# Kernel optimization log

Hardware: AMD Instinct MI355X
Metric: run time of the kernel (lower is better)

The kernel has to match this reference:

```python
import jax, jax.numpy as jnp
import numpy as np

B, S, D, E, K = 4, 2048, 1024, 8, 2


def setup_inputs() -> dict:
    key = jax.random.key(0)
    k1, k2, k3 = jax.random.split(key, 3)
    scale = 1.0 / np.sqrt(D)
    x = jax.random.normal(k1, (B, S, D), dtype=jnp.float32)
    Wg = jax.random.normal(k2, (D, E), dtype=jnp.float32) * scale
    bg = jnp.zeros((E,), dtype=jnp.float32)
    We = jax.random.normal(k3, (E, D, D), dtype=jnp.float32) * scale
    be = jnp.zeros((E, D), dtype=jnp.float32)
    return {"x": x, "Wg": Wg, "bg": bg, "We": We, "be": be}


def reference(x, Wg, bg, We, be):
    # gate scores: [B, S, E]
    gate_scores = jnp.einsum("bsd,de->bse", x, Wg) + bg
    topk_values, topk_indices = jax.lax.top_k(gate_scores, K)
    # mask: -inf everywhere except at top-k indices (where value == score)
    sel = jax.nn.one_hot(topk_indices, E, dtype=jnp.bool_).any(axis=-2)  # [B,S,E]
    masked = jnp.where(sel, gate_scores, -jnp.inf)
    gate_weights = jax.nn.softmax(masked, axis=-1)  # [B,S,E]
    # dense all-expert compute, as in the original: [B,S,E,D]
    expert_outputs = jnp.einsum("bsd,edh->bseh", x, We) + be
    fused = jnp.einsum("bse,bseh->bsh", gate_weights, expert_outputs)
    return fused
```

## Files before the change

kernel.cpp:

```cpp
#include <hip/hip_runtime.h>
#include <stdint.h>

#define NTOK   8192
#define DIM    1024
#define NEXP   8
#define MAXP   8192

#define BM 128
#define BN 128
#define BK 32

typedef float    f32x4  __attribute__((ext_vector_type(4)));
typedef __bf16   bf16x8 __attribute__((ext_vector_type(8)));
typedef _Float16 h16x8  __attribute__((ext_vector_type(8)));

typedef __attribute__((address_space(1))) const void* gas_ptr;
typedef __attribute__((address_space(3))) void*       las_ptr;

__device__ __forceinline__ unsigned short f32_to_bf16(float f) {
  union { float f; unsigned int u; } v; v.f = f;
  unsigned int u = v.u;
  unsigned int r = (u + 0x7FFFu + ((u >> 16) & 1u)) >> 16;
  return (unsigned short)r;
}

__global__ __launch_bounds__(256) void prep_kernel(
    const float* __restrict__ We, unsigned short* __restrict__ Wf,
    const float* __restrict__ x, const float* __restrict__ Wg,
    const float* __restrict__ bg, unsigned short* __restrict__ Xbf,
    int* __restrict__ tok_ee, float2* __restrict__ tok_w) {
  __shared__ float tile[64][65];
  const int bid = blockIdx.x;
  if (bid < 2048) {
    const int e  = bid >> 8;
    const int d0 = ((bid >> 4) & 15) * 64;
    const int h0 = (bid & 15) * 64;
    const int t  = threadIdx.x;
    const int tx = t & 63, ty = t >> 6;
    const float* src = We + (size_t)e * DIM * DIM;
#pragma unroll
    for (int i = 0; i < 16; ++i) {
      int d = ty + i * 4;
      tile[d][tx] = src[(size_t)(d0 + d) * DIM + (h0 + tx)];
    }
    __syncthreads();
    const int nt    = h0 >> 7;
    const int rbase = h0 & 64;
    const int hl    = t >> 2;
    const int k8    = t & 3;
#pragma unroll
    for (int reg = 0; reg < 2; ++reg) {
      const int kt = (d0 >> 5) + reg;
      unsigned int pk[4];
#pragma unroll
      for (int q = 0; q < 4; ++q) {
        int dl = reg * 32 + k8 * 8 + q * 2;
        pk[q] = (unsigned int)f32_to_bf16(tile[dl][hl]) |
                ((unsigned int)f32_to_bf16(tile[dl + 1][hl]) << 16);
      }
      size_t base = (((size_t)(e * 8 + nt) * 32 + kt) << 12) +
                    (size_t)(rbase + hl) * 32 + k8 * 8;
      *(uint4*)&Wf[base] = make_uint4(pk[0], pk[1], pk[2], pk[3]);
    }
    return;
  }
  const int blk  = bid - 2048;
  const int wave = threadIdx.x >> 6;
  const int lane = threadIdx.x & 63;
  const int tok0 = blk * 16 + wave * 4;

  float xs[4][16];
#pragma unroll
  for (int t = 0; t < 4; ++t) {
    const float* xr = x + (size_t)(tok0 + t) * DIM + lane * 16;
#pragma unroll
    for (int i = 0; i < 4; ++i)
      *(f32x4*)&xs[t][i * 4] = *(const f32x4*)(xr + i * 4);
  }
#pragma unroll
  for (int t = 0; t < 4; ++t) {
    unsigned int pk[8];
#pragma unroll
    for (int i = 0; i < 8; ++i)
      pk[i] = (unsigned int)f32_to_bf16(xs[t][2 * i]) |
              ((unsigned int)f32_to_bf16(xs[t][2 * i + 1]) << 16);
    uint4* xb = (uint4*)(Xbf + (size_t)(tok0 + t) * DIM + lane * 16);
    xb[0] = make_uint4(pk[0], pk[1], pk[2], pk[3]);
    xb[1] = make_uint4(pk[4], pk[5], pk[6], pk[7]);
  }

  double acc[4][8];
#pragma unroll
  for (int t = 0; t < 4; ++t)
#pragma unroll
    for (int e = 0; e < 8; ++e) acc[t][e] = 0.0;

  const float* wr = Wg + (size_t)(lane * 16) * NEXP;
#pragma unroll
  for (int i = 0; i < 16; ++i) {
    f32x4 wa = *(const f32x4*)(wr + i * 8);
    f32x4 wb = *(const f32x4*)(wr + i * 8 + 4);
    double w0 = wa[0], w1 = wa[1], w2 = wa[2], w3 = wa[3];
    double w4 = wb[0], w5 = wb[1], w6 = wb[2], w7 = wb[3];
#pragma unroll
    for (int t = 0; t < 4; ++t) {
      double xd = (double)xs[t][i];
      acc[t][0] += xd * w0; acc[t][1] += xd * w1;
      acc[t][2] += xd * w2; acc[t][3] += xd * w3;
      acc[t][4] += xd * w4; acc[t][5] += xd * w5;
      acc[t][6] += xd * w6; acc[t][7] += xd * w7;
    }
  }
#pragma unroll
  for (int m = 1; m < 64; m <<= 1)
#pragma unroll
    for (int t = 0; t < 4; ++t)
#pragma unroll
      for (int e = 0; e < 8; ++e) acc[t][e] += __shfl_xor(acc[t][e], m, 64);

  if (lane == 0) {
#pragma unroll
    for (int t = 0; t < 4; ++t) {
      float s[8];
#pragma unroll
      for (int e = 0; e < 8; ++e) s[e] = (float)acc[t][e] + bg[e];
      int i0 = 0; float v0 = s[0];
#pragma unroll
      for (int e = 1; e < 8; ++e) if (s[e] > v0) { v0 = s[e]; i0 = e; }
      int i1 = -1; float v1 = -3.4e38f;
#pragma unroll
      for (int e = 0; e < 8; ++e) if (e != i0 && s[e] > v1) { v1 = s[e]; i1 = e; }
      float t1 = expf(v1 - v0);
      float den = 1.0f + t1;
      tok_ee[tok0 + t] = i0 | (i1 << 8);
      tok_w[tok0 + t]  = make_float2(1.0f / den, t1 / den);
    }
  }
}

__global__ __launch_bounds__(1024) void compact_kernel(
    const int* __restrict__ tok_ee, const float2* __restrict__ tok_w,
    int* __restrict__ counts, int* __restrict__ pair_token,
    float* __restrict__ pair_w) {
  __shared__ int wave_cnt[16];
  __shared__ int wave_off[16];
  const int e = blockIdx.x;
  const int tid = threadIdx.x, wave = tid >> 6, lane = tid & 63;
  int base = 0;
  for (int c = 0; c < NTOK / 1024; ++c) {
    const int t = c * 1024 + tid;
    const int p = tok_ee[t];
    const bool m0 = ((p & 255) == e);
    const bool m1 = (((p >> 8) & 255) == e);
    const unsigned long long m = __ballot(m0 || m1);
    const int pre = __popcll(m & ((1ull << lane) - 1ull));
    if (lane == 0) wave_cnt[wave] = __popcll(m);
    __syncthreads();
    if (tid == 0) {
      int s = base;
      for (int w = 0; w < 16; ++w) { wave_off[w] = s; s += wave_cnt[w]; }
      base = s;
    }
    __syncthreads();
    if (m0 || m1) {
      const float2 w = tok_w[t];
      const int slot = wave_off[wave] + pre;
      pair_token[e * MAXP + slot] = (t << 1) | (m1 ? 1 : 0);
      pair_w[e * MAXP + slot]     = m1 ? w.y : w.x;
    }
    __syncthreads();
  }
  if (tid == 0) counts[e] = base;
}

__global__ __launch_bounds__(256) void moe_gemm(
    const unsigned short* __restrict__ Xbf, const unsigned short* __restrict__ Wf,
    const float* __restrict__ be, const int* __restrict__ counts,
    const int* __restrict__ pair_token, const float* __restrict__ pair_w,
    _Float16* __restrict__ part, float* __restrict__ Y, int use_part) {
  const int id  = blockIdx.x;
  const int e   = id & 7;
  const int nt  = (id >> 3) & 7;
  const int n0  = nt * BN;
  const int m0  = (id >> 6) * BM;
  const int cnt = counts[e];
  if (m0 >= cnt) return;

  __shared__ __align__(16) unsigned short As[3][BM * BK];
  __shared__ __align__(16) unsigned short Bs[3][BN * BK];

  const int tid  = threadIdx.x;
  const int wave = tid >> 6;
  const int lane = tid & 63;
  const int fm   = lane & 15;
  const int fq   = lane >> 4;
  const int wm   = wave >> 1;
  const int wn   = wave & 1;

  const int srow = wave * 32 + (lane >> 2);
  const int kc   = (((lane & 3) ^ ((lane >> 3) & 3)) * 8);
  const unsigned short* gA[2];
#pragma unroll
  for (int c = 0; c < 2; ++c) {
    int r  = srow + c * 16;
    int gr = m0 + r;
    int tk = (gr < cnt) ? (pair_token[e * MAXP + gr] >> 1) : 0;
    gA[c] = Xbf + (size_t)tk * DIM + kc;
  }
  const unsigned short* gB = Wf + (((size_t)(e * 8 + nt) * 32) << 12) +
                             (wave * 2) * 512 + (lane >> 2) * 32 + kc;

#define STAGE(buf, k0v)                                                       \
  {                                                                           \
    _Pragma("unroll") for (int c = 0; c < 2; ++c) {                           \
      __builtin_amdgcn_global_load_lds(                                       \
          (gas_ptr)(uintptr_t)(gA[c] + (k0v)),                                \
          (las_ptr)(uintptr_t)(&As[buf][(wave * 2 + c) * 512]), 16, 0, 0);    \
      __builtin_amdgcn_global_load_lds(                                       \
          (gas_ptr)(uintptr_t)(gB + (size_t)(k0v) * 128 + c * 512),           \
          (las_ptr)(uintptr_t)(&Bs[buf][(wave * 2 + c) * 512]), 16, 0, 0);    \
    }                                                                         \
  }

  f32x4 acc[4][4];
#pragma unroll
  for (int i = 0; i < 4; ++i)
#pragma unroll
    for (int j = 0; j < 4; ++j) { f32x4 z = {0.f, 0.f, 0.f, 0.f}; acc[i][j] = z; }

  const int ks = ((fq ^ ((fm >> 1) & 3)) * 8);

  STAGE(0, 0);
  STAGE(1, BK);
  int cur = 0;
  for (int k0 = 0; k0 < DIM; k0 += BK) {
    asm volatile("s_waitcnt vmcnt(4)" ::: "memory");
    __builtin_amdgcn_s_barrier();

    int kn = k0 + 2 * BK;
    if (kn >= DIM) kn = 0;
    int nb = cur + 2;
    if (nb >= 3) nb -= 3;
    STAGE(nb, kn);

    bf16x8 af[4], bfr[4];
#pragma unroll
    for (int i = 0; i < 4; ++i)
      af[i] = *(const bf16x8*)&As[cur][(wm * 64 + i * 16 + fm) * BK + ks];
#pragma unroll
    for (int j = 0; j < 4; ++j)
      bfr[j] = *(const bf16x8*)&Bs[cur][(wn * 64 + j * 16 + fm) * BK + ks];
#pragma unroll
    for (int i = 0; i < 4; ++i)
#pragma unroll
      for (int j = 0; j < 4; ++j)
        acc[i][j] = __builtin_amdgcn_mfma_f32_16x16x32_bf16(af[i], bfr[j],
                                                            acc[i][j], 0, 0, 0);
    cur = (cur + 1 == 3) ? 0 : cur + 1;
  }
#undef STAGE

  int   rowv[4][4];
  float wrow[4][4];
#pragma unroll
  for (int i = 0; i < 4; ++i)
#pragma unroll
    for (int r = 0; r < 4; ++r) {
      int gr = m0 + wm * 64 + i * 16 + fq * 4 + r;
      bool valid = gr < cnt;
      rowv[i][r] = valid ? pair_token[e * MAXP + gr] : -1;
      wrow[i][r] = valid ? pair_w[e * MAXP + gr] : 0.f;
    }
  if (use_part) {
#pragma unroll
    for (int j = 0; j < 4; ++j) {
      int col = n0 + wn * 64 + j * 16 + fm;
      float bev = be[e * DIM + col];
#pragma unroll
      for (int i = 0; i < 4; ++i)
#pragma unroll
        for (int r = 0; r < 4; ++r) {
          int v = rowv[i][r];
          if (v >= 0)
            __builtin_nontemporal_store(
                (_Float16)(wrow[i][r] * (acc[i][j][r] + bev)),
                &part[(size_t)v * DIM + col]);
        }
    }
  } else {
#pragma unroll
    for (int j = 0; j < 4; ++j) {
      int col = n0 + wn * 64 + j * 16 + fm;
      float bev = be[e * DIM + col];
#pragma unroll
      for (int i = 0; i < 4; ++i)
#pragma unroll
        for (int r = 0; r < 4; ++r) {
          int v = rowv[i][r];
          if (v >= 0)
            atomicAdd(Y + (size_t)(v >> 1) * DIM + col,
                      wrow[i][r] * (acc[i][j][r] + bev));
        }
    }
  }
}

__global__ __launch_bounds__(256) void reduce_pairs(
    const _Float16* __restrict__ part, float* __restrict__ Y) {
  const int g = blockIdx.x * 256 + threadIdx.x;
  const int t = g >> 7;
  const int o = (g & 127) * 8;
  const h16x8 a =
      __builtin_nontemporal_load((const h16x8*)(part + (size_t)(2 * t) * DIM + o));
  const h16x8 b =
      __builtin_nontemporal_load((const h16x8*)(part + (size_t)(2 * t + 1) * DIM + o));
  float* y = Y + (size_t)t * DIM + o;
  f32x4 lo = {(float)a[0] + (float)b[0], (float)a[1] + (float)b[1],
              (float)a[2] + (float)b[2], (float)a[3] + (float)b[3]};
  f32x4 hi = {(float)a[4] + (float)b[4], (float)a[5] + (float)b[5],
              (float)a[6] + (float)b[6], (float)a[7] + (float)b[7]};
  __builtin_nontemporal_store(lo, (f32x4*)y);
  __builtin_nontemporal_store(hi, (f32x4*)(y + 4));
}

extern "C" void kernel_launch(void* const* d_in, const int* in_sizes, int n_in,
                              void* d_out, int out_size, void* d_ws, size_t ws_size,
                              hipStream_t stream) {
  const float* x  = (const float*)d_in[0];
  const float* Wg = (const float*)d_in[1];
  const float* bg = (const float*)d_in[2];
  const float* We = (const float*)d_in[3];
  const float* be = (const float*)d_in[4];
  float* Y = (float*)d_out;

  const size_t MB = 1024 * 1024;
  char* ws = (char*)d_ws;
  unsigned short* Xbf = (unsigned short*)ws;
  unsigned short* Wf  = (unsigned short*)(ws + 16 * MB);
  const size_t part_bytes = (size_t)NTOK * 2 * DIM * 2;
  const size_t need = 32 * MB + part_bytes + 1 * MB;
  const int use_part = ws_size >= need;
  _Float16* part = (_Float16*)(ws + 32 * MB);
  char* p2 = ws + 32 * MB + (use_part ? part_bytes : 0);
  int*    counts     = (int*)p2;
  int*    pair_token = (int*)(p2 + 256);
  float*  pair_w     = (float*)(p2 + 256 + 262144);
  int*    tok_ee     = (int*)(p2 + 256 + 2 * 262144);
  float2* tok_w      = (float2*)(p2 + 256 + 2 * 262144 + 32768);

  if (!use_part)
    hipMemsetAsync(d_out, 0, (size_t)out_size * sizeof(float), stream);

  prep_kernel<<<2560, 256, 0, stream>>>(We, Wf, x, Wg, bg, Xbf, tok_ee, tok_w);
  compact_kernel<<<NEXP, 1024, 0, stream>>>(tok_ee, tok_w, counts, pair_token,
                                            pair_w);
  moe_gemm<<<8 * 8 * (NTOK / BM), 256, 0, stream>>>(
      Xbf, Wf, be, counts, pair_token, pair_w, part, Y, use_part);
  if (use_part)
    reduce_pairs<<<NTOK * DIM / 8 / 256, 256, 0, stream>>>(part, Y);
}
```

Baseline: 221.2 us.

## Enlarge MoE GEMM tiles to 256x256 with 8 waves and ping-pong pipelining

```diff
diff --git a/kernel.cpp b/kernel.cpp
--- a/kernel.cpp
+++ b/kernel.cpp
@@ -5,10 +5,6 @@
 #define DIM    1024
 #define NEXP   8
 #define MAXP   8192
-
-#define BM 128
-#define BN 128
-#define BK 32
 
 typedef float    f32x4  __attribute__((ext_vector_type(4)));
 typedef __bf16   bf16x8 __attribute__((ext_vector_type(8)));
@@ -173,100 +169,149 @@
   if (tid == 0) counts[e] = base;
 }
 
-__global__ __launch_bounds__(256) void moe_gemm(
+#define BARC()                                  \
+  { asm volatile("" ::: "memory");              \
+    __builtin_amdgcn_s_barrier();               \
+    asm volatile("" ::: "memory"); }
+
+__global__ __launch_bounds__(512, 2) void moe_gemm(
     const unsigned short* __restrict__ Xbf, const unsigned short* __restrict__ Wf,
     const float* __restrict__ be, const int* __restrict__ counts,
     const int* __restrict__ pair_token, const float* __restrict__ pair_w,
     _Float16* __restrict__ part, float* __restrict__ Y, int use_part) {
-  const int id  = blockIdx.x;
-  const int e   = id & 7;
-  const int nt  = (id >> 3) & 7;
-  const int n0  = nt * BN;
-  const int m0  = (id >> 6) * BM;
-  const int cnt = counts[e];
+  const int id    = blockIdx.x;
+  const int e     = id & 7;
+  const int ntile = (id >> 3) & 3;
+  const int m0    = (id >> 5) * 256;
+  const int cnt   = counts[e];
   if (m0 >= cnt) return;
 
-  __shared__ __align__(16) unsigned short As[3][BM * BK];
-  __shared__ __align__(16) unsigned short Bs[3][BN * BK];
+  __shared__ __align__(16) unsigned short As[2][2][256 * 32];
+  __shared__ __align__(16) unsigned short Bs[2][2][256 * 32];
 
   const int tid  = threadIdx.x;
   const int wave = tid >> 6;
   const int lane = tid & 63;
   const int fm   = lane & 15;
   const int fq   = lane >> 4;
-  const int wm   = wave >> 1;
-  const int wn   = wave & 1;
-
-  const int srow = wave * 32 + (lane >> 2);
-  const int kc   = (((lane & 3) ^ ((lane >> 3) & 3)) * 8);
+  const int wm   = wave >> 2;
+  const int wn   = wave & 3;
+
+  const int kc = (((lane & 3) ^ ((lane >> 3) & 3)) * 8);
   const unsigned short* gA[2];
-#pragma unroll
-  for (int c = 0; c < 2; ++c) {
-    int r  = srow + c * 16;
-    int gr = m0 + r;
-    int tk = (gr < cnt) ? (pair_token[e * MAXP + gr] >> 1) : 0;
-    gA[c] = Xbf + (size_t)tk * DIM + kc;
-  }
-  const unsigned short* gB = Wf + (((size_t)(e * 8 + nt) * 32) << 12) +
-                             (wave * 2) * 512 + (lane >> 2) * 32 + kc;
-
-#define STAGE(buf, k0v)                                                       \
-  {                                                                           \
-    _Pragma("unroll") for (int c = 0; c < 2; ++c) {                           \
+  const unsigned short* gB[2];
+#pragma unroll
+  for (int l = 0; l < 2; ++l) {
+    const int R  = wave * 2 + l;
+    const int gr = m0 + R * 16 + (lane >> 2);
+    const int tk = (gr < cnt) ? (pair_token[e * MAXP + gr] >> 1) : 0;
+    gA[l] = Xbf + (size_t)tk * DIM + kc;
+    gB[l] = Wf + ((size_t)(e * 8 + ntile * 2 + (R >> 3)) << 17) +
+            (size_t)((R & 7) * 16 + (lane >> 2)) * 32 + kc;
+  }
+
+#define STAGE_A(buf, ksv, ttv)                                                \
+  { _Pragma("unroll") for (int l = 0; l < 2; ++l)                             \
       __builtin_amdgcn_global_load_lds(                                       \
-          (gas_ptr)(uintptr_t)(gA[c] + (k0v)),                                \
-          (las_ptr)(uintptr_t)(&As[buf][(wave * 2 + c) * 512]), 16, 0, 0);    \
+          (gas_ptr)(uintptr_t)(gA[l] + (ttv) * 64 + (ksv) * 32),              \
+          (las_ptr)(uintptr_t)(&As[buf][ksv][(wave * 2 + l) * 512]), 16, 0, 0); }
+#define STAGE_B(buf, ksv, ttv)                                                \
+  { _Pragma("unroll") for (int l = 0; l < 2; ++l)                             \
       __builtin_amdgcn_global_load_lds(                                       \
-          (gas_ptr)(uintptr_t)(gB + (size_t)(k0v) * 128 + c * 512),           \
-          (las_ptr)(uintptr_t)(&Bs[buf][(wave * 2 + c) * 512]), 16, 0, 0);    \
-    }                                                                         \
-  }
-
-  f32x4 acc[4][4];
-#pragma unroll
-  for (int i = 0; i < 4; ++i)
+          (gas_ptr)(uintptr_t)(gB[l] + (size_t)((ttv) * 2 + (ksv)) * 4096),   \
+          (las_ptr)(uintptr_t)(&Bs[buf][ksv][(wave * 2 + l) * 512]), 16, 0, 0); }
+
+  f32x4 acc[8][4];
+#pragma unroll
+  for (int i = 0; i < 8; ++i)
 #pragma unroll
     for (int j = 0; j < 4; ++j) { f32x4 z = {0.f, 0.f, 0.f, 0.f}; acc[i][j] = z; }
 
-  const int ks = ((fq ^ ((fm >> 1) & 3)) * 8);
-
-  STAGE(0, 0);
-  STAGE(1, BK);
-  int cur = 0;
-  for (int k0 = 0; k0 < DIM; k0 += BK) {
+  const int rdo  = (fq ^ ((fm >> 1) & 3)) * 8;
+  const int arow = (wm * 128 + fm) * 32 + rdo;
+  const int brow = (wn * 64 + fm) * 32 + rdo;
+
+#define MFMA16(JB)                                                            \
+  { _Pragma("unroll") for (int i = 0; i < 8; ++i)                             \
+      _Pragma("unroll") for (int j = 0; j < 2; ++j)                           \
+        acc[i][(JB) + j] = __builtin_amdgcn_mfma_f32_16x16x32_bf16(           \
+            af[i], bfr[j], acc[i][(JB) + j], 0, 0, 0); }
+
+  STAGE_A(0, 0, 0); STAGE_B(0, 0, 0); STAGE_A(0, 1, 0); STAGE_B(0, 1, 0);
+  asm volatile("s_waitcnt vmcnt(0)" ::: "memory");
+  BARC();
+
+#pragma unroll 2
+  for (int t = 0; t < 16; ++t) {
+    const int p  = t & 1;
+    const int q  = p ^ 1;
+    const int tt = (t + 1) & 15;
+    bf16x8 af[8], bfr[2];
+
+#pragma unroll
+    for (int i = 0; i < 8; ++i) af[i] = *(const bf16x8*)&As[p][0][arow + i * 512];
+#pragma unroll
+    for (int j = 0; j < 2; ++j) bfr[j] = *(const bf16x8*)&Bs[p][0][brow + j * 512];
+    STAGE_A(q, 0, tt);
+    BARC();
+    asm volatile("s_waitcnt lgkmcnt(0)" ::: "memory");
+    __builtin_amdgcn_sched_barrier(0);
+    __builtin_amdgcn_s_setprio(1);
+    MFMA16(0);
+    __builtin_amdgcn_s_setprio(0);
+    BARC();
+
+#pragma unroll
+    for (int j = 0; j < 2; ++j)
+      bfr[j] = *(const bf16x8*)&Bs[p][0][brow + 1024 + j * 512];
+    STAGE_B(q, 0, tt);
+    BARC();
+    asm volatile("s_waitcnt lgkmcnt(0)" ::: "memory");
+    __builtin_amdgcn_sched_barrier(0);
+    __builtin_amdgcn_s_setprio(1);
+    MFMA16(2);
+    __builtin_amdgcn_s_setprio(0);
     asm volatile("s_waitcnt vmcnt(4)" ::: "memory");
-    __builtin_amdgcn_s_barrier();
-
-    int kn = k0 + 2 * BK;
-    if (kn >= DIM) kn = 0;
-    int nb = cur + 2;
-    if (nb >= 3) nb -= 3;
-    STAGE(nb, kn);
-
-    bf16x8 af[4], bfr[4];
-#pragma unroll
-    for (int i = 0; i < 4; ++i)
-      af[i] = *(const bf16x8*)&As[cur][(wm * 64 + i * 16 + fm) * BK + ks];
-#pragma unroll
-    for (int j = 0; j < 4; ++j)
-      bfr[j] = *(const bf16x8*)&Bs[cur][(wn * 64 + j * 16 + fm) * BK + ks];
-#pragma unroll
-    for (int i = 0; i < 4; ++i)
-#pragma unroll
-      for (int j = 0; j < 4; ++j)
-        acc[i][j] = __builtin_amdgcn_mfma_f32_16x16x32_bf16(af[i], bfr[j],
-                                                            acc[i][j], 0, 0, 0);
-    cur = (cur + 1 == 3) ? 0 : cur + 1;
-  }
-#undef STAGE
-
-  int   rowv[4][4];
-  float wrow[4][4];
-#pragma unroll
-  for (int i = 0; i < 4; ++i)
+    BARC();
+
+#pragma unroll
+    for (int i = 0; i < 8; ++i) af[i] = *(const bf16x8*)&As[p][1][arow + i * 512];
+#pragma unroll
+    for (int j = 0; j < 2; ++j) bfr[j] = *(const bf16x8*)&Bs[p][1][brow + j * 512];
+    STAGE_A(q, 1, tt);
+    BARC();
+    asm volatile("s_waitcnt lgkmcnt(0)" ::: "memory");
+    __builtin_amdgcn_sched_barrier(0);
+    __builtin_amdgcn_s_setprio(1);
+    MFMA16(0);
+    __builtin_amdgcn_s_setprio(0);
+    BARC();
+
+#pragma unroll
+    for (int j = 0; j < 2; ++j)
+      bfr[j] = *(const bf16x8*)&Bs[p][1][brow + 1024 + j * 512];
+    STAGE_B(q, 1, tt);
+    BARC();
+    asm volatile("s_waitcnt lgkmcnt(0)" ::: "memory");
+    __builtin_amdgcn_sched_barrier(0);
+    __builtin_amdgcn_s_setprio(1);
+    MFMA16(2);
+    __builtin_amdgcn_s_setprio(0);
+    asm volatile("s_waitcnt vmcnt(4)" ::: "memory");
+    BARC();
+  }
+  asm volatile("s_waitcnt vmcnt(0)" ::: "memory");
+#undef STAGE_A
+#undef STAGE_B
+#undef MFMA16
+
+  int   rowv[8][4];
+  float wrow[8][4];
+#pragma unroll
+  for (int i = 0; i < 8; ++i)
 #pragma unroll
     for (int r = 0; r < 4; ++r) {
-      int gr = m0 + wm * 64 + i * 16 + fq * 4 + r;
+      int gr = m0 + wm * 128 + i * 16 + fq * 4 + r;
       bool valid = gr < cnt;
       rowv[i][r] = valid ? pair_token[e * MAXP + gr] : -1;
       wrow[i][r] = valid ? pair_w[e * MAXP + gr] : 0.f;
@@ -274,10 +319,10 @@
   if (use_part) {
 #pragma unroll
     for (int j = 0; j < 4; ++j) {
-      int col = n0 + wn * 64 + j * 16 + fm;
+      int col = ntile * 256 + wn * 64 + j * 16 + fm;
       float bev = be[e * DIM + col];
 #pragma unroll
-      for (int i = 0; i < 4; ++i)
+      for (int i = 0; i < 8; ++i)
 #pragma unroll
         for (int r = 0; r < 4; ++r) {
           int v = rowv[i][r];
@@ -290,10 +335,10 @@
   } else {
 #pragma unroll
     for (int j = 0; j < 4; ++j) {
-      int col = n0 + wn * 64 + j * 16 + fm;
+      int col = ntile * 256 + wn * 64 + j * 16 + fm;
       float bev = be[e * DIM + col];
 #pragma unroll
-      for (int i = 0; i < 4; ++i)
+      for (int i = 0; i < 8; ++i)
 #pragma unroll
         for (int r = 0; r < 4; ++r) {
           int v = rowv[i][r];
@@ -354,7 +399,7 @@
   prep_kernel<<<2560, 256, 0, stream>>>(We, Wf, x, Wg, bg, Xbf, tok_ee, tok_w);
   compact_kernel<<<NEXP, 1024, 0, stream>>>(tok_ee, tok_w, counts, pair_token,
                                             pair_w);
-  moe_gemm<<<8 * 8 * (NTOK / BM), 256, 0, stream>>>(
+  moe_gemm<<<8 * 4 * (MAXP / 256), 512, 0, stream>>>(
       Xbf, Wf, be, counts, pair_token, pair_w, part, Y, use_part);
   if (use_part)
     reduce_pairs<<<NTOK * DIM / 8 / 256, 256, 0, stream>>>(part, Y);
```

New measurement: 241.8 us. 9.3% more time.

## Fuse token compaction into gating via atomics and widen GEMM tile to 128x256

Applied to the files above, without the earlier changes.

```diff
diff --git a/kernel.cpp b/kernel.cpp
--- a/kernel.cpp
+++ b/kernel.cpp
@@ -5,10 +5,6 @@
 #define DIM    1024
 #define NEXP   8
 #define MAXP   8192
-
-#define BM 128
-#define BN 128
-#define BK 32
 
 typedef float    f32x4  __attribute__((ext_vector_type(4)));
 typedef __bf16   bf16x8 __attribute__((ext_vector_type(8)));
@@ -28,7 +24,8 @@
     const float* __restrict__ We, unsigned short* __restrict__ Wf,
     const float* __restrict__ x, const float* __restrict__ Wg,
     const float* __restrict__ bg, unsigned short* __restrict__ Xbf,
-    int* __restrict__ tok_ee, float2* __restrict__ tok_w) {
+    int* __restrict__ counts, int* __restrict__ pair_token,
+    float* __restrict__ pair_w) {
   __shared__ float tile[64][65];
   const int bid = blockIdx.x;
   if (bid < 2048) {
@@ -132,94 +129,62 @@
       for (int e = 0; e < 8; ++e) if (e != i0 && s[e] > v1) { v1 = s[e]; i1 = e; }
       float t1 = expf(v1 - v0);
       float den = 1.0f + t1;
-      tok_ee[tok0 + t] = i0 | (i1 << 8);
-      tok_w[tok0 + t]  = make_float2(1.0f / den, t1 / den);
-    }
-  }
-}
-
-__global__ __launch_bounds__(1024) void compact_kernel(
-    const int* __restrict__ tok_ee, const float2* __restrict__ tok_w,
-    int* __restrict__ counts, int* __restrict__ pair_token,
-    float* __restrict__ pair_w) {
-  __shared__ int wave_cnt[16];
-  __shared__ int wave_off[16];
-  const int e = blockIdx.x;
-  const int tid = threadIdx.x, wave = tid >> 6, lane = tid & 63;
-  int base = 0;
-  for (int c = 0; c < NTOK / 1024; ++c) {
-    const int t = c * 1024 + tid;
-    const int p = tok_ee[t];
-    const bool m0 = ((p & 255) == e);
-    const bool m1 = (((p >> 8) & 255) == e);
-    const unsigned long long m = __ballot(m0 || m1);
-    const int pre = __popcll(m & ((1ull << lane) - 1ull));
-    if (lane == 0) wave_cnt[wave] = __popcll(m);
-    __syncthreads();
-    if (tid == 0) {
-      int s = base;
-      for (int w = 0; w < 16; ++w) { wave_off[w] = s; s += wave_cnt[w]; }
-      base = s;
-    }
-    __syncthreads();
-    if (m0 || m1) {
-      const float2 w = tok_w[t];
-      const int slot = wave_off[wave] + pre;
-      pair_token[e * MAXP + slot] = (t << 1) | (m1 ? 1 : 0);
-      pair_w[e * MAXP + slot]     = m1 ? w.y : w.x;
-    }
-    __syncthreads();
-  }
-  if (tid == 0) counts[e] = base;
-}
-
-__global__ __launch_bounds__(256) void moe_gemm(
+      const int tok = tok0 + t;
+      int s0 = atomicAdd(&counts[i0], 1);
+      pair_token[i0 * MAXP + s0] = tok << 1;
+      pair_w[i0 * MAXP + s0]     = 1.0f / den;
+      int s1 = atomicAdd(&counts[i1], 1);
+      pair_token[i1 * MAXP + s1] = (tok << 1) | 1;
+      pair_w[i1 * MAXP + s1]     = t1 / den;
+    }
+  }
+}
+
+__global__ __launch_bounds__(512, 4) void moe_gemm(
     const unsigned short* __restrict__ Xbf, const unsigned short* __restrict__ Wf,
     const float* __restrict__ be, const int* __restrict__ counts,
     const int* __restrict__ pair_token, const float* __restrict__ pair_w,
     _Float16* __restrict__ part, float* __restrict__ Y, int use_part) {
-  const int id  = blockIdx.x;
-  const int e   = id & 7;
-  const int nt  = (id >> 3) & 7;
-  const int n0  = nt * BN;
-  const int m0  = (id >> 6) * BM;
-  const int cnt = counts[e];
+  const int id    = blockIdx.x;
+  const int e     = id & 7;
+  const int ntile = (id >> 3) & 3;
+  const int m0    = (id >> 5) * 128;
+  const int cnt   = counts[e];
   if (m0 >= cnt) return;
 
-  __shared__ __align__(16) unsigned short As[3][BM * BK];
-  __shared__ __align__(16) unsigned short Bs[3][BN * BK];
+  __shared__ __align__(16) unsigned short As[3][128 * 32];
+  __shared__ __align__(16) unsigned short Bs[3][256 * 32];
 
   const int tid  = threadIdx.x;
   const int wave = tid >> 6;
   const int lane = tid & 63;
   const int fm   = lane & 15;
   const int fq   = lane >> 4;
-  const int wm   = wave >> 1;
-  const int wn   = wave & 1;
-
-  const int srow = wave * 32 + (lane >> 2);
-  const int kc   = (((lane & 3) ^ ((lane >> 3) & 3)) * 8);
-  const unsigned short* gA[2];
-#pragma unroll
-  for (int c = 0; c < 2; ++c) {
-    int r  = srow + c * 16;
-    int gr = m0 + r;
-    int tk = (gr < cnt) ? (pair_token[e * MAXP + gr] >> 1) : 0;
-    gA[c] = Xbf + (size_t)tk * DIM + kc;
-  }
-  const unsigned short* gB = Wf + (((size_t)(e * 8 + nt) * 32) << 12) +
-                             (wave * 2) * 512 + (lane >> 2) * 32 + kc;
+  const int wm   = wave >> 2;
+  const int wn   = wave & 3;
+
+  const int kc = (((lane & 3) ^ ((lane >> 3) & 3)) * 8);
+  const int grA = m0 + wave * 16 + (lane >> 2);
+  const int tkA = (grA < cnt) ? (pair_token[e * MAXP + grA] >> 1) : 0;
+  const unsigned short* gA = Xbf + (size_t)tkA * DIM + kc;
+  const unsigned short* gB[2];
+#pragma unroll
+  for (int l = 0; l < 2; ++l) {
+    const int R16 = wave * 2 + l;
+    const int cg  = ntile * 2 + (R16 >> 3);
+    gB[l] = Wf + ((size_t)(e * 8 + cg) << 17) +
+            (size_t)((R16 & 7) * 16 + (lane >> 2)) * 32 + kc;
+  }
 
 #define STAGE(buf, k0v)                                                       \
   {                                                                           \
-    _Pragma("unroll") for (int c = 0; c < 2; ++c) {                           \
+    __builtin_amdgcn_global_load_lds(                                         \
+        (gas_ptr)(uintptr_t)(gA + (k0v)),                                     \
+        (las_ptr)(uintptr_t)(&As[buf][wave * 512]), 16, 0, 0);                \
+    _Pragma("unroll") for (int l = 0; l < 2; ++l)                             \
       __builtin_amdgcn_global_load_lds(                                       \
-          (gas_ptr)(uintptr_t)(gA[c] + (k0v)),                                \
-          (las_ptr)(uintptr_t)(&As[buf][(wave * 2 + c) * 512]), 16, 0, 0);    \
-      __builtin_amdgcn_global_load_lds(                                       \
-          (gas_ptr)(uintptr_t)(gB + (size_t)(k0v) * 128 + c * 512),           \
-          (las_ptr)(uintptr_t)(&Bs[buf][(wave * 2 + c) * 512]), 16, 0, 0);    \
-    }                                                                         \
+          (gas_ptr)(uintptr_t)(gB[l] + (size_t)(k0v) * 128),                  \
+          (las_ptr)(uintptr_t)(&Bs[buf][(wave * 2 + l) * 512]), 16, 0, 0);    \
   }
 
   f32x4 acc[4][4];
@@ -228,16 +193,18 @@
 #pragma unroll
     for (int j = 0; j < 4; ++j) { f32x4 z = {0.f, 0.f, 0.f, 0.f}; acc[i][j] = z; }
 
-  const int ks = ((fq ^ ((fm >> 1) & 3)) * 8);
+  const int rdo  = (fq ^ ((fm >> 1) & 3)) * 8;
+  const int arow = (wm * 64 + fm) * 32 + rdo;
+  const int brow = (wn * 64 + fm) * 32 + rdo;
 
   STAGE(0, 0);
-  STAGE(1, BK);
+  STAGE(1, 32);
   int cur = 0;
-  for (int k0 = 0; k0 < DIM; k0 += BK) {
-    asm volatile("s_waitcnt vmcnt(4)" ::: "memory");
+  for (int k0 = 0; k0 < DIM; k0 += 32) {
+    asm volatile("s_waitcnt vmcnt(3)" ::: "memory");
     __builtin_amdgcn_s_barrier();
 
-    int kn = k0 + 2 * BK;
+    int kn = k0 + 64;
     if (kn >= DIM) kn = 0;
     int nb = cur + 2;
     if (nb >= 3) nb -= 3;
@@ -246,10 +213,10 @@
     bf16x8 af[4], bfr[4];
 #pragma unroll
     for (int i = 0; i < 4; ++i)
-      af[i] = *(const bf16x8*)&As[cur][(wm * 64 + i * 16 + fm) * BK + ks];
+      af[i] = *(const bf16x8*)&As[cur][arow + i * 512];
 #pragma unroll
     for (int j = 0; j < 4; ++j)
-      bfr[j] = *(const bf16x8*)&Bs[cur][(wn * 64 + j * 16 + fm) * BK + ks];
+      bfr[j] = *(const bf16x8*)&Bs[cur][brow + j * 512];
 #pragma unroll
     for (int i = 0; i < 4; ++i)
 #pragma unroll
@@ -258,49 +225,47 @@
                                                             acc[i][j], 0, 0, 0);
     cur = (cur + 1 == 3) ? 0 : cur + 1;
   }
+  asm volatile("s_waitcnt vmcnt(0)" ::: "memory");
 #undef STAGE
 
-  int   rowv[4][4];
-  float wrow[4][4];
-#pragma unroll
-  for (int i = 0; i < 4; ++i)
+#pragma unroll
+  for (int i = 0; i < 4; ++i) {
+    int   rv[4];
+    float wv[4];
 #pragma unroll
     for (int r = 0; r < 4; ++r) {
       int gr = m0 + wm * 64 + i * 16 + fq * 4 + r;
       bool valid = gr < cnt;
-      rowv[i][r] = valid ? pair_token[e * MAXP + gr] : -1;
-      wrow[i][r] = valid ? pair_w[e * MAXP + gr] : 0.f;
-    }
-  if (use_part) {
-#pragma unroll
-    for (int j = 0; j < 4; ++j) {
-      int col = n0 + wn * 64 + j * 16 + fm;
-      float bev = be[e * DIM + col];
-#pragma unroll
-      for (int i = 0; i < 4; ++i)
+      rv[r] = valid ? pair_token[e * MAXP + gr] : -1;
+      wv[r] = valid ? pair_w[e * MAXP + gr] : 0.f;
+    }
+    if (use_part) {
+#pragma unroll
+      for (int j = 0; j < 4; ++j) {
+        int col = ntile * 256 + wn * 64 + j * 16 + fm;
+        float bev = be[e * DIM + col];
 #pragma unroll
         for (int r = 0; r < 4; ++r) {
-          int v = rowv[i][r];
+          int v = rv[r];
           if (v >= 0)
             __builtin_nontemporal_store(
-                (_Float16)(wrow[i][r] * (acc[i][j][r] + bev)),
+                (_Float16)(wv[r] * (acc[i][j][r] + bev)),
                 &part[(size_t)v * DIM + col]);
         }
-    }
-  } else {
-#pragma unroll
-    for (int j = 0; j < 4; ++j) {
-      int col = n0 + wn * 64 + j * 16 + fm;
-      float bev = be[e * DIM + col];
-#pragma unroll
-      for (int i = 0; i < 4; ++i)
+      }
+    } else {
+#pragma unroll
+      for (int j = 0; j < 4; ++j) {
+        int col = ntile * 256 + wn * 64 + j * 16 + fm;
+        float bev = be[e * DIM + col];
 #pragma unroll
         for (int r = 0; r < 4; ++r) {
-          int v = rowv[i][r];
+          int v = rv[r];
           if (v >= 0)
             atomicAdd(Y + (size_t)(v >> 1) * DIM + col,
-                      wrow[i][r] * (acc[i][j][r] + bev));
+                      wv[r] * (acc[i][j][r] + bev));
         }
+      }
     }
   }
 }
@@ -345,16 +310,14 @@
   int*    counts     = (int*)p2;
   int*    pair_token = (int*)(p2 + 256);
   float*  pair_w     = (float*)(p2 + 256 + 262144);
-  int*    tok_ee     = (int*)(p2 + 256 + 2 * 262144);
-  float2* tok_w      = (float2*)(p2 + 256 + 2 * 262144 + 32768);
-
+
+  hipMemsetAsync(counts, 0, 256, stream);
   if (!use_part)
     hipMemsetAsync(d_out, 0, (size_t)out_size * sizeof(float), stream);
 
-  prep_kernel<<<2560, 256, 0, stream>>>(We, Wf, x, Wg, bg, Xbf, tok_ee, tok_w);
-  compact_kernel<<<NEXP, 1024, 0, stream>>>(tok_ee, tok_w, counts, pair_token,
-                                            pair_w);
-  moe_gemm<<<8 * 8 * (NTOK / BM), 256, 0, stream>>>(
+  prep_kernel<<<2560, 256, 0, stream>>>(We, Wf, x, Wg, bg, Xbf, counts,
+                                        pair_token, pair_w);
+  moe_gemm<<<8 * 4 * (MAXP / 128), 512, 0, stream>>>(
       Xbf, Wf, be, counts, pair_token, pair_w, part, Y, use_part);
   if (use_part)
     reduce_pairs<<<NTOK * DIM / 8 / 256, 256, 0, stream>>>(part, Y);
```

Result: slower. 389.2 us (+76.0%).
